# Performance work log

Measured on AMD Instinct MI355X. Metric: run time of the kernel, lower is better.

The kernel has to match this reference:

```python
import jax, jax.numpy as jnp
import numpy as np

B, S, D = 4, 2048, 1152
H, KVH, HD = 16, 4, 64
SW = 1792
NEG = jnp.float32(-1e9)


def setup_inputs() -> dict:
    key = jax.random.key(0)
    ks = jax.random.split(key, 6)
    x = jax.random.normal(ks[0], (B, S, D), jnp.float32)
    s = 0.02
    wq = jax.random.normal(ks[1], (H * HD, D), jnp.float32) * s
    wk = jax.random.normal(ks[2], (KVH * HD, D), jnp.float32) * s
    wv = jax.random.normal(ks[3], (KVH * HD, D), jnp.float32) * s
    wo = jax.random.normal(ks[4], (D, H * HD), jnp.float32) * s
    # rotary freqs: theta=10000, standard llama-style
    inv = 1.0 / (10000.0 ** (np.arange(0, HD, 2, dtype=np.float32) / HD))
    t = np.arange(S, dtype=np.float32)
    fr = np.outer(t, inv)  # [S, HD//2]
    freqs_cos = jnp.asarray(np.cos(fr), jnp.float32)
    freqs_sin = jnp.asarray(np.sin(fr), jnp.float32)
    positions = jnp.arange(S, dtype=jnp.int32)
    # sliding-window causal additive mask: attend j iff 0 <= i-j < SW
    i = jnp.arange(S)[:, None]
    j = jnp.arange(S)[None, :]
    allowed = (j <= i) & (i - j < SW)
    mask = jnp.where(allowed, jnp.float32(0.0), NEG)
    cache_k = jnp.zeros((B, SW, KVH, HD), jnp.float32)
    cache_v = jnp.zeros((B, SW, KVH, HD), jnp.float32)
    return {"x": x, "wq": wq, "wk": wk, "wv": wv, "wo": wo,
            "freqs_cos": freqs_cos, "freqs_sin": freqs_sin, "mask": mask,
            "cache_k": cache_k, "cache_v": cache_v, "positions": positions}


def _rope(t, cos, sin):
    # t: [B,S,h,HD]; complex multiply on (even, odd) pairs
    tr = t.reshape(t.shape[:-1] + (HD // 2, 2))
    a, b = tr[..., 0], tr[..., 1]
    c = cos[None, :, None, :]
    s = sin[None, :, None, :]
    out = jnp.stack([a * c - b * s, a * s + b * c], axis=-1)
    return out.reshape(t.shape)


def reference(x, wq, wk, wv, wo, freqs_cos, freqs_sin, mask, cache_k, cache_v, positions):
    bsz, seqlen, _ = x.shape
    xq = jnp.einsum('bsd,ed->bse', x, wq).reshape(bsz, seqlen, H, HD)
    xk = jnp.einsum('bsd,ed->bse', x, wk).reshape(bsz, seqlen, KVH, HD)
    xv = jnp.einsum('bsd,ed->bse', x, wv).reshape(bsz, seqlen, KVH, HD)
    xq = _rope(xq, freqs_cos, freqs_sin)
    xk = _rope(xk, freqs_cos, freqs_sin)
    # circular-buffer cache scatter (last SW tokens, modulo indexing)
    idx = positions[-SW:] % SW
    new_ck = cache_k.at[:, idx].set(xk[:, -SW:])
    new_cv = cache_v.at[:, idx].set(xv[:, -SW:])
    # GQA: expand kv heads (repeat_interleave on head dim)
    rep = H // KVH
    key = jnp.repeat(xk, rep, axis=2)   # [B,S,H,HD]
    value = jnp.repeat(xv, rep, axis=2)
    q = xq.transpose(0, 2, 1, 3)        # [B,H,S,HD]
    k = key.transpose(0, 2, 1, 3)
    v = value.transpose(0, 2, 1, 3)
    scale = 1.0 / jnp.sqrt(jnp.float32(HD))
    scores = jnp.einsum('bhqd,bhkd->bhqk', q, k) * scale + mask[None, None]
    probs = jax.nn.softmax(scores, axis=-1)
    out = jnp.einsum('bhqk,bhkd->bhqd', probs, v)
    out = out.transpose(0, 2, 1, 3).reshape(bsz, seqlen, H * HD)
    out = jnp.einsum('bse,de->bsd', out, wo)
    return out, new_ck, new_cv
```

## Files before the change

kernel.cpp:

```cpp
#include <hip/hip_runtime.h>
#include <cstdint>
#include <cstddef>


typedef unsigned short u16;
typedef unsigned int   u32;
typedef __attribute__((ext_vector_type(8))) short bf16x8;
typedef __attribute__((ext_vector_type(4))) float f32x4;

#define AS1(p) ((const __attribute__((address_space(1))) void*)(p))
#define AS3(p) ((__attribute__((address_space(3))) void*)(p))

__device__ __forceinline__ u16 f2bf(float f) {
  u32 u = __float_as_uint(f);
  u += 0x7fffu + ((u >> 16) & 1u);
  return (u16)(u >> 16);
}
__device__ __forceinline__ float bf2f(u32 x) { return __uint_as_float(x << 16); }
__device__ __forceinline__ f32x4 mfma16(bf16x8 a, bf16x8 b, f32x4 c) {
  return __builtin_amdgcn_mfma_f32_16x16x32_bf16(a, b, c, 0, 0, 0);
}
__device__ __forceinline__ u32 cvtpk_bf16(float lo, float hi) {
  u32 r;
  asm("v_cvt_pk_bf16_f32 %0, %1, %2" : "=v"(r) : "v"(lo), "v"(hi));
  return r;
}

__global__ __launch_bounds__(256) void cvt5_kernel(const float* __restrict__ x,
                                                   const float* __restrict__ wq,
                                                   const float* __restrict__ wk,
                                                   const float* __restrict__ wv,
                                                   const float* __restrict__ wo,
                                                   u16* __restrict__ xb,
                                                   u16* __restrict__ wqkvb,
                                                   u16* __restrict__ wob) {
  int i = blockIdx.x * 256 + threadIdx.x;
  const float* in; u16* out; int off; float sc = 1.0f;
  if (i < 2359296)      { in = x;  out = xb;                  off = i; }
  else if (i < 2654208) { in = wq; out = wqkvb;               off = i - 2359296;
                          sc = 0.18033688011112042f; }
  else if (i < 2727936) { in = wk; out = wqkvb + 1024 * 1152; off = i - 2654208; }
  else if (i < 2801664) { in = wv; out = wqkvb + 1280 * 1152; off = i - 2727936; }
  else                  { in = wo; out = wob;                 off = i - 2801664; }
  float4 v = ((const float4*)in)[off];
  uint2 o;
  o.x = (u32)f2bf(v.x * sc) | ((u32)f2bf(v.y * sc) << 16);
  o.y = (u32)f2bf(v.z * sc) | ((u32)f2bf(v.w * sc) << 16);
  ((uint2*)out)[off] = o;
}

template<int BF16_OUT>
__global__ __launch_bounds__(256) void gemm_bt(const u16* __restrict__ A,
                                               const u16* __restrict__ B,
                                               void* __restrict__ C,
                                               int M, int N, int K, int NT) {
  __shared__ u16 As[128][64];
  __shared__ u16 Bs[128][64];
  const int tid  = threadIdx.x;
  const int w    = tid >> 6, lane = tid & 63;
  const int l15  = lane & 15, hi4 = lane >> 4;
  const int lid  = blockIdx.x;
  const int k_   = lid >> 3;
  const int by   = (lid & 7) + 8 * (k_ / NT);
  const int bx   = k_ % NT;
  const int m0   = by * 128, n0 = bx * 128;
  const int wr   = w >> 1, wc = w & 1;

  const int srow = lane >> 3;
  const int scol = ((lane & 7) ^ srow) << 3;
  const u16* Ab = A + (size_t)(m0 + w * 32 + srow) * K + scol;
  const u16* Bb = B + (size_t)(n0 + w * 32 + srow) * K + scol;
  u16* AsDst = &As[w * 32][0];
  u16* BsDst = &Bs[w * 32][0];

  const int swz = (l15 & 7) << 4;
  const int c0  = (((hi4 * 16)      ^ swz) >> 1);
  const int c1  = (((64 + hi4 * 16) ^ swz) >> 1);
  const u16* aRd = &As[wr * 64 + l15][0];
  const u16* bRd = &Bs[wc * 64 + l15][0];

  f32x4 acc[4][4] = {};

  for (int kk = 0; kk < K; kk += 64) {
#pragma unroll
    for (int q = 0; q < 4; q++) {
      __builtin_amdgcn_global_load_lds(AS1(Ab + kk + (size_t)q * 8 * K),
                                       AS3(AsDst + q * 8 * 64), 16, 0, 0);
      __builtin_amdgcn_global_load_lds(AS1(Bb + kk + (size_t)q * 8 * K),
                                       AS3(BsDst + q * 8 * 64), 16, 0, 0);
    }
    __syncthreads();
#pragma unroll
    for (int ks = 0; ks < 2; ks++) {
      const int cc = ks ? c1 : c0;
      bf16x8 af[4], bfr[4];
#pragma unroll
      for (int t = 0; t < 4; t++) af[t]  = *(const bf16x8*)(aRd + t * 16 * 64 + cc);
#pragma unroll
      for (int t = 0; t < 4; t++) bfr[t] = *(const bf16x8*)(bRd + t * 16 * 64 + cc);
#pragma unroll
      for (int mi = 0; mi < 4; mi++)
#pragma unroll
        for (int ni = 0; ni < 4; ni++)
          acc[mi][ni] = mfma16(af[mi], bfr[ni], acc[mi][ni]);
    }
    __syncthreads();
  }

#pragma unroll
  for (int mi = 0; mi < 4; mi++) {
#pragma unroll
    for (int r = 0; r < 4; r++) {
      int row = m0 + wr * 64 + mi * 16 + hi4 * 4 + r;
      size_t base = (size_t)row * N + n0 + wc * 64 + l15;
#pragma unroll
      for (int ni = 0; ni < 4; ni++) {
        float v = acc[mi][ni][r];
        if (BF16_OUT) ((u16*)C)[base + ni * 16] = f2bf(v);
        else          ((float*)C)[base + ni * 16] = v;
      }
    }
  }
}

__global__ __launch_bounds__(256) void ropev_kernel(u16* __restrict__ buf,
                                                    float* __restrict__ kcache,
                                                    u16* __restrict__ vT,
                                                    float* __restrict__ ncv,
                                                    const float* __restrict__ cosT,
                                                    const float* __restrict__ sinT) {
  __shared__ u16 tile[64][65];
  if (blockIdx.x < 4096) {
    int idx = blockIdx.x * 256 + threadIdx.x;
    int m = idx >> 7, p = idx & 127;
    int s = m & 2047, b = m >> 11;
    int hh = p & 31;
    u32* bp = (u32*)buf + (size_t)m * 768 + 512 + p;
    u32 pk = *bp;
    float a  = bf2f(pk & 0xffffu), bb = bf2f(pk >> 16);
    float c  = cosT[s * 32 + hh],  sn = sinT[s * 32 + hh];
    float o0 = a * c - bb * sn;
    float o1 = a * sn + bb * c;
    *bp = (u32)f2bf(o0) | ((u32)f2bf(o1) << 16);
    if (s >= 256) {
      int pc = (s < 1792) ? s : s - 1792;
      float2* cp = (float2*)(kcache + (size_t)(b * 1792 + pc) * 256 + 2 * p);
      *cp = make_float2(o0, o1);
    }
  } else {
    int bi = blockIdx.x - 4096;
    int s0 = (bi & 31) * 64, kvh = (bi >> 5) & 3, b = bi >> 7;
    int t = threadIdx.x;
    int r = t >> 2, cc = (t & 3) * 16;
    const u16* src = buf + (size_t)(b * 2048 + s0 + r) * 1536 + 1280 + kvh * 64 + cc;
    uint4 v0 = *(const uint4*)src;
    uint4 v1 = *(const uint4*)(src + 8);
    u16 vals[16];
    *(uint4*)&vals[0] = v0;
    *(uint4*)&vals[8] = v1;
    int s = s0 + r;
    if (s >= 256) {
      int pc = (s < 1792) ? s : s - 1792;
      float* dst = ncv + (size_t)(b * 1792 + pc) * 256 + kvh * 64 + cc;
#pragma unroll
      for (int i = 0; i < 16; i += 4) {
        float4 f = make_float4(bf2f(vals[i]), bf2f(vals[i + 1]),
                               bf2f(vals[i + 2]), bf2f(vals[i + 3]));
        *(float4*)(dst + i) = f;
      }
    }
#pragma unroll
    for (int i = 0; i < 16; i++) tile[cc + i][r] = vals[i];
    __syncthreads();
    u16 ov[16];
#pragma unroll
    for (int i = 0; i < 16; i++) ov[i] = tile[r][cc + i];
    u16* dst2 = vT + (size_t)((b * 4 + kvh) * 64 + r) * 2048 + s0 + cc;
    *(uint4*)dst2 = *(uint4*)&ov[0];
    *(uint4*)(dst2 + 8) = *(uint4*)&ov[8];
  }
}

__global__ __launch_bounds__(256) void attn_kernel(const u16* __restrict__ qkv,
                                                   const u16* __restrict__ vT,
                                                   u16* __restrict__ attnb,
                                                   const float* __restrict__ cosT,
                                                   const float* __restrict__ sinT) {
  __shared__ __align__(16) u16 Kbuf[2][64][64];
  __shared__ __align__(16) u16 Vbuf[2][64][64];
  const int tid = threadIdx.x;
  const int w = tid >> 6, lane = tid & 63;
  const int l15 = lane & 15, hi4 = lane >> 4;

  const int lid = blockIdx.x;
  const int g   = lid & 7;
  const int t_  = lid >> 3;
  const int u_  = t_ >> 1, v_ = t_ & 1;
  const int c   = v_ ? u_ : (63 - u_);
  const int rr  = 2 * g + v_;
  const int kvh = rr & 3, b = rr >> 2;
  const int i0  = 32 * c;
  const int h   = kvh * 4 + w;

  const u16* qbase = qkv + (size_t)(b * 2048) * 1536 + h * 64;
  const u16* kbase = qkv + (size_t)(b * 2048) * 1536 + 1024 + kvh * 64;
  const u16* vbase = vT + (size_t)((b * 4 + kvh) * 64) * 2048;

  bf16x8 qa[2][2];
  {
    const u16* qp = qbase + (size_t)(i0 + l15) * 1536 + hi4 * 8;
#pragma unroll
    for (int m = 0; m < 2; m++) {
      const int s = i0 + m * 16 + l15;
#pragma unroll
      for (int ki = 0; ki < 2; ki++) {
        bf16x8 qv = *(const bf16x8*)(qp + m * 16 * 1536 + ki * 32);
        const int hh0 = ki * 16 + hi4 * 4;
        float4 cs = *(const float4*)(cosT + s * 32 + hh0);
        float4 sn = *(const float4*)(sinT + s * 32 + hh0);
        u32 wds[4];
        {
          float a = bf2f((u16)qv[0]), bb2 = bf2f((u16)qv[1]);
          wds[0] = cvtpk_bf16(a * cs.x - bb2 * sn.x, a * sn.x + bb2 * cs.x);
        }
        {
          float a = bf2f((u16)qv[2]), bb2 = bf2f((u16)qv[3]);
          wds[1] = cvtpk_bf16(a * cs.y - bb2 * sn.y, a * sn.y + bb2 * cs.y);
        }
        {
          float a = bf2f((u16)qv[4]), bb2 = bf2f((u16)qv[5]);
          wds[2] = cvtpk_bf16(a * cs.z - bb2 * sn.z, a * sn.z + bb2 * cs.z);
        }
        {
          float a = bf2f((u16)qv[6]), bb2 = bf2f((u16)qv[7]);
          wds[3] = cvtpk_bf16(a * cs.w - bb2 * sn.w, a * sn.w + bb2 * cs.w);
        }
        qa[m][ki] = *(const bf16x8*)&wds[0];
      }
    }
  }

  bf16x8 ones;
#pragma unroll
  for (int i = 0; i < 8; i++) ones[i] = (short)0x3F80;

  f32x4 o[2][4] = {};
  f32x4 ol[2] = {};

  const int srow = lane >> 3;
  const int ssl  = (lane & 7) ^ srow;

#define STAGE(J0, BS)                                                                     \
  do {                                                                                    \
    _Pragma("unroll")                                                                     \
    for (int q = 0; q < 2; q++) {                                                         \
      const int row = 32 * q + 8 * w + srow;                                              \
      __builtin_amdgcn_global_load_lds(AS1(kbase + (size_t)((J0) + row) * 1536 + ssl * 8),\
                                       AS3(&Kbuf[BS][32 * q + 8 * w][0]), 16, 0, 0);      \
      __builtin_amdgcn_global_load_lds(AS1(vbase + (size_t)row * 2048 + (J0) + ssl * 8),  \
                                       AS3(&Vbuf[BS][32 * q + 8 * w][0]), 16, 0, 0);      \
    }                                                                                     \
  } while (0)

  int jstart = i0 - 1791;
  if (jstart < 0) jstart = 0;
  jstart &= ~63;
  const int jend = i0 + 32;
  const int ntiles = (jend - jstart + 63) >> 6;

  STAGE(jstart, 0);
  if (ntiles > 1) STAGE(jstart + 64, 1);

  for (int t = 0; t < ntiles; t++) {
    const int j0 = jstart + 64 * t;
    if (t + 1 < ntiles) asm volatile("s_waitcnt vmcnt(4)" ::: "memory");
    else                asm volatile("s_waitcnt vmcnt(0)" ::: "memory");
    __builtin_amdgcn_s_barrier();
    __builtin_amdgcn_sched_barrier(0);

    const u16* Kb = &Kbuf[t & 1][0][0];
    const u16* Vb = &Vbuf[t & 1][0][0];

    bf16x8 kf[2][4];
#pragma unroll
    for (int nt = 0; nt < 4; nt++)
#pragma unroll
      for (int ki = 0; ki < 2; ki++)
        kf[ki][nt] = *(const bf16x8*)(Kb + (nt * 16 + l15) * 64 +
                                      (((ki * 4 + hi4) ^ (l15 & 7)) << 3));

    u32 vfd[4][2][4];
#pragma unroll
    for (int tt = 0; tt < 4; tt++) {
      const int row = tt * 16 + l15;
      const u16* Vrow = Vb + row * 64;
      const int rs = row & 7;
      const int inner = (hi4 & 1) * 4;
      const int h1 = hi4 >> 1;
#pragma unroll
      for (int kbp = 0; kbp < 2; kbp++) {
        int us0 = (((4 * kbp + h1)     ^ rs) << 3) + inner;
        int us1 = (((4 * kbp + 2 + h1) ^ rs) << 3) + inner;
        uint2 lo = *(const uint2*)(Vrow + us0);
        uint2 hi = *(const uint2*)(Vrow + us1);
        vfd[tt][kbp][0] = lo.x; vfd[tt][kbp][1] = lo.y;
        vfd[tt][kbp][2] = hi.x; vfd[tt][kbp][3] = hi.y;
      }
    }
    asm volatile("s_waitcnt lgkmcnt(0)" ::: "memory");
    __builtin_amdgcn_sched_barrier(0);
    __builtin_amdgcn_s_barrier();
    if (t + 2 < ntiles) STAGE(j0 + 128, t & 1);

    __builtin_amdgcn_s_setprio(1);
    const bool fast = (j0 + 63 <= i0) && (i0 + 31 - j0 < 1792);
#pragma unroll
    for (int m = 0; m < 2; m++) {
      __align__(16) u32 pkb[8];
#pragma unroll
      for (int nt = 0; nt < 4; nt++) {
        f32x4 s = {0.f, 0.f, 0.f, 0.f};
        s = mfma16(kf[0][nt], qa[m][0], s);
        s = mfma16(kf[1][nt], qa[m][1], s);
        float p[4];
        if (fast) {
#pragma unroll
          for (int r = 0; r < 4; r++) p[r] = __builtin_amdgcn_exp2f(s[r]);
        } else {
#pragma unroll
          for (int r = 0; r < 4; r++) {
            const int j = j0 + nt * 16 + hi4 * 4 + r;
            const int i = i0 + m * 16 + l15;
            p[r] = (j <= i && i - j < 1792) ? __builtin_amdgcn_exp2f(s[r]) : 0.f;
          }
        }
        pkb[nt * 2]     = cvtpk_bf16(p[0], p[1]);
        pkb[nt * 2 + 1] = cvtpk_bf16(p[2], p[3]);
      }
      bf16x8 pa0 = *(const bf16x8*)&pkb[0];
      bf16x8 pa1 = *(const bf16x8*)&pkb[4];
#pragma unroll
      for (int tt = 0; tt < 4; tt++) {
        o[m][tt] = mfma16(pa0, *(const bf16x8*)&vfd[tt][0][0], o[m][tt]);
        o[m][tt] = mfma16(pa1, *(const bf16x8*)&vfd[tt][1][0], o[m][tt]);
      }
      ol[m] = mfma16(pa0, ones, ol[m]);
      ol[m] = mfma16(pa1, ones, ol[m]);
    }
    __builtin_amdgcn_s_setprio(0);
  }
#undef STAGE

  u16* op = attnb + (size_t)(b * 2048 + i0 + hi4 * 4) * 1024 + h * 64 + l15;
#pragma unroll
  for (int m = 0; m < 2; m++)
#pragma unroll
    for (int r = 0; r < 4; r++) {
      float inv = 1.0f / ol[m][r];
#pragma unroll
      for (int tt = 0; tt < 4; tt++)
        op[(size_t)(m * 16 + r) * 1024 + 16 * tt] = f2bf(o[m][tt][r] * inv);
    }
}

extern "C" void kernel_launch(void* const* d_in, const int* in_sizes, int n_in,
                              void* d_out, int out_size, void* d_ws, size_t ws_size,
                              hipStream_t stream) {
  const float* x  = (const float*)d_in[0];
  const float* wq = (const float*)d_in[1];
  const float* wk = (const float*)d_in[2];
  const float* wv = (const float*)d_in[3];
  const float* wo = (const float*)d_in[4];
  const float* fc = (const float*)d_in[5];
  const float* fs = (const float*)d_in[6];

  float* out = (float*)d_out;
  float* nck = out + 9437184;
  float* ncv = nck + 1835008;

  char* ws = (char*)d_ws;
  u16* attnb = (u16*)(ws);
  u16* xb    = (u16*)(ws);
  u16* wqkvb = (u16*)(ws + 18874368);
  u16* wob   = (u16*)(ws + 22413312);
  u16* qkv   = (u16*)(ws + 24772608);
  u16* vT    = (u16*)(ws + 49938432);

  cvt5_kernel<<<12096, 256, 0, stream>>>(x, wq, wk, wv, wo, xb, wqkvb, wob);

  gemm_bt<1><<<768, 256, 0, stream>>>(xb, wqkvb, qkv, 8192, 1536, 1152, 12);

  ropev_kernel<<<4608, 256, 0, stream>>>(qkv, nck, vT, ncv, fc, fs);

  attn_kernel<<<1024, 256, 0, stream>>>(qkv, vT, attnb, fc, fs);

  gemm_bt<0><<<576, 256, 0, stream>>>(attnb, wob, out, 8192, 1152, 1024, 9);
}
```

Before: 183.8 us.

## Permute V transpose layout for 128-bit LDS reads and rework attention scheduling

The V-transpose kernel now writes key positions in a permuted order, so the attention kernel can read each V fragment with one swizzled 128-bit LDS load instead of paired 64-bit loads. The Q softmax scale moves from the weight conversion into the RoPE cos/sin factors, which removes a multiply from the conversion kernel. The K/V prefetch for tile t+2 is moved after the compute, guarded by a single barrier, and the explicit lgkmcnt wait is dropped. The block-to-tile mapping is also reordered, which changes the load-balancing order, and the later prefetch may reduce overlap of loads with compute.

```diff
diff --git a/kernel.cpp b/kernel.cpp
--- a/kernel.cpp
+++ b/kernel.cpp
@@ -35,17 +35,16 @@
                                                    u16* __restrict__ wqkvb,
                                                    u16* __restrict__ wob) {
   int i = blockIdx.x * 256 + threadIdx.x;
-  const float* in; u16* out; int off; float sc = 1.0f;
+  const float* in; u16* out; int off;
   if (i < 2359296)      { in = x;  out = xb;                  off = i; }
-  else if (i < 2654208) { in = wq; out = wqkvb;               off = i - 2359296;
-                          sc = 0.18033688011112042f; }
+  else if (i < 2654208) { in = wq; out = wqkvb;               off = i - 2359296; }
   else if (i < 2727936) { in = wk; out = wqkvb + 1024 * 1152; off = i - 2654208; }
   else if (i < 2801664) { in = wv; out = wqkvb + 1280 * 1152; off = i - 2727936; }
   else                  { in = wo; out = wob;                 off = i - 2801664; }
   float4 v = ((const float4*)in)[off];
   uint2 o;
-  o.x = (u32)f2bf(v.x * sc) | ((u32)f2bf(v.y * sc) << 16);
-  o.y = (u32)f2bf(v.z * sc) | ((u32)f2bf(v.w * sc) << 16);
+  o.x = (u32)f2bf(v.x) | ((u32)f2bf(v.y) << 16);
+  o.y = (u32)f2bf(v.z) | ((u32)f2bf(v.w) << 16);
   ((uint2*)out)[off] = o;
 }
 
@@ -174,7 +173,12 @@
     __syncthreads();
     u16 ov[16];
 #pragma unroll
-    for (int i = 0; i < 16; i++) ov[i] = tile[r][cc + i];
+    for (int i = 0; i < 16; i++) {
+      int p = cc + i;
+      int pg = p & 31, e = pg & 7, g = pg >> 3;
+      int key = (p & ~31) + ((e < 4) ? (4 * g + e) : (16 + 4 * g + (e - 4)));
+      ov[i] = tile[r][key];
+    }
     u16* dst2 = vT + (size_t)((b * 4 + kvh) * 64 + r) * 2048 + s0 + cc;
     *(uint4*)dst2 = *(uint4*)&ov[0];
     *(uint4*)(dst2 + 8) = *(uint4*)&ov[8];
@@ -192,20 +196,19 @@
   const int w = tid >> 6, lane = tid & 63;
   const int l15 = lane & 15, hi4 = lane >> 4;
 
-  const int lid = blockIdx.x;
-  const int g   = lid & 7;
-  const int t_  = lid >> 3;
-  const int u_  = t_ >> 1, v_ = t_ & 1;
-  const int c   = v_ ? u_ : (63 - u_);
-  const int rr  = 2 * g + v_;
-  const int kvh = rr & 3, b = rr >> 2;
-  const int i0  = 32 * c;
-  const int h   = kvh * 4 + w;
+  const int lid  = blockIdx.x;
+  const int wgid = (lid & 7) * 128 + (lid >> 3);
+  const int gx   = wgid & 63;
+  const int rr   = wgid >> 6;
+  const int kvh  = rr & 3, b = rr >> 2;
+  const int i0   = 32 * (63 - gx);
+  const int h    = kvh * 4 + w;
 
   const u16* qbase = qkv + (size_t)(b * 2048) * 1536 + h * 64;
   const u16* kbase = qkv + (size_t)(b * 2048) * 1536 + 1024 + kvh * 64;
   const u16* vbase = vT + (size_t)((b * 4 + kvh) * 64) * 2048;
 
+  const float qs = 0.18033688011112042f;
   bf16x8 qa[2][2];
   {
     const u16* qp = qbase + (size_t)(i0 + l15) * 1536 + hi4 * 8;
@@ -218,6 +221,8 @@
         const int hh0 = ki * 16 + hi4 * 4;
         float4 cs = *(const float4*)(cosT + s * 32 + hh0);
         float4 sn = *(const float4*)(sinT + s * 32 + hh0);
+        cs.x *= qs; cs.y *= qs; cs.z *= qs; cs.w *= qs;
+        sn.x *= qs; sn.y *= qs; sn.z *= qs; sn.w *= qs;
         u32 wds[4];
         {
           float a = bf2f((u16)qv[0]), bb2 = bf2f((u16)qv[1]);
@@ -289,28 +294,15 @@
         kf[ki][nt] = *(const bf16x8*)(Kb + (nt * 16 + l15) * 64 +
                                       (((ki * 4 + hi4) ^ (l15 & 7)) << 3));
 
-    u32 vfd[4][2][4];
+    bf16x8 vf[2][4];
 #pragma unroll
     for (int tt = 0; tt < 4; tt++) {
       const int row = tt * 16 + l15;
-      const u16* Vrow = Vb + row * 64;
-      const int rs = row & 7;
-      const int inner = (hi4 & 1) * 4;
-      const int h1 = hi4 >> 1;
-#pragma unroll
-      for (int kbp = 0; kbp < 2; kbp++) {
-        int us0 = (((4 * kbp + h1)     ^ rs) << 3) + inner;
-        int us1 = (((4 * kbp + 2 + h1) ^ rs) << 3) + inner;
-        uint2 lo = *(const uint2*)(Vrow + us0);
-        uint2 hi = *(const uint2*)(Vrow + us1);
-        vfd[tt][kbp][0] = lo.x; vfd[tt][kbp][1] = lo.y;
-        vfd[tt][kbp][2] = hi.x; vfd[tt][kbp][3] = hi.y;
-      }
-    }
-    asm volatile("s_waitcnt lgkmcnt(0)" ::: "memory");
-    __builtin_amdgcn_sched_barrier(0);
-    __builtin_amdgcn_s_barrier();
-    if (t + 2 < ntiles) STAGE(j0 + 128, t & 1);
+#pragma unroll
+      for (int kbp = 0; kbp < 2; kbp++)
+        vf[kbp][tt] = *(const bf16x8*)(Vb + row * 64 +
+                                       (((kbp * 4 + hi4) ^ (l15 & 7)) << 3));
+    }
 
     __builtin_amdgcn_s_setprio(1);
     const bool fast = (j0 + 63 <= i0) && (i0 + 31 - j0 < 1792);
@@ -327,10 +319,10 @@
 #pragma unroll
           for (int r = 0; r < 4; r++) p[r] = __builtin_amdgcn_exp2f(s[r]);
         } else {
+          const int i = i0 + m * 16 + l15;
 #pragma unroll
           for (int r = 0; r < 4; r++) {
             const int j = j0 + nt * 16 + hi4 * 4 + r;
-            const int i = i0 + m * 16 + l15;
             p[r] = (j <= i && i - j < 1792) ? __builtin_amdgcn_exp2f(s[r]) : 0.f;
           }
         }
@@ -341,13 +333,17 @@
       bf16x8 pa1 = *(const bf16x8*)&pkb[4];
 #pragma unroll
       for (int tt = 0; tt < 4; tt++) {
-        o[m][tt] = mfma16(pa0, *(const bf16x8*)&vfd[tt][0][0], o[m][tt]);
-        o[m][tt] = mfma16(pa1, *(const bf16x8*)&vfd[tt][1][0], o[m][tt]);
+        o[m][tt] = mfma16(pa0, vf[0][tt], o[m][tt]);
+        o[m][tt] = mfma16(pa1, vf[1][tt], o[m][tt]);
       }
       ol[m] = mfma16(pa0, ones, ol[m]);
       ol[m] = mfma16(pa1, ones, ol[m]);
     }
     __builtin_amdgcn_s_setprio(0);
+
+    __builtin_amdgcn_s_barrier();
+    __builtin_amdgcn_sched_barrier(0);
+    if (t + 2 < ntiles) STAGE(j0 + 128, t & 1);
   }
 #undef STAGE
 
```

Measured after the change: 152.2 us. -17.2%, faster.
